# Optimization experiments

Measured on AMD Instinct MI355X. Metric: run time of the kernel, lower is better.

Reference implementation:

```python
import jax, jax.numpy as jnp
from jax import lax
import numpy as np

N, K, QK, W = 10, 10, 150, 128
D = 256
HID = 100
CHANS = [1, 16, 32, 64, 128, 256]
STRIDES = [2, 2, 1, 1, 1]
ITERS = 3
BN_EPS = 1e-5


def setup_inputs() -> dict:
    key = jax.random.key(0)
    ks = jax.random.split(key, 12)
    inp = {
        "support": jax.random.normal(ks[0], (N, K, 1, W, W), jnp.float32),
        "query": jax.random.normal(ks[1], (QK, 1, W, W), jnp.float32),
    }
    for i in range(5):
        inp[f"conv_w{i}"] = jax.random.normal(ks[2 + i], (CHANS[i + 1], CHANS[i], 3, 3), jnp.float32) * 0.05
        inp[f"bn_g{i}"] = jnp.ones((CHANS[i + 1],), jnp.float32)
        inp[f"bn_b{i}"] = jnp.zeros((CHANS[i + 1],), jnp.float32)
    inp["trans_w"] = jax.random.normal(ks[8], (D, D), jnp.float32) * 0.05
    inp["trans_b"] = jnp.zeros((D,), jnp.float32)
    inp["bil_w"] = jax.random.normal(ks[9], (HID, D, D), jnp.float32) * 0.02
    inp["score_w"] = jax.random.normal(ks[10], (1, HID), jnp.float32) * 0.1
    inp["score_b"] = jnp.zeros((1,), jnp.float32)
    return inp


def _block(x, w, g, b, s):
    # Conv2d(k=3, pad=1, stride=s, no bias) -> BatchNorm(eval: mean=0, var=1) -> ReLU -> MaxPool2d(2)
    x = lax.conv_general_dilated(x, w, (s, s), ((1, 1), (1, 1)),
                                 dimension_numbers=('NCHW', 'OIHW', 'NCHW'))
    scale = (g / jnp.sqrt(1.0 + BN_EPS))[None, :, None, None]
    x = jax.nn.relu(x * scale + b[None, :, None, None])
    return lax.reduce_window(x, -jnp.inf, lax.max, (1, 1, 2, 2), (1, 1, 2, 2), 'VALID')


def reference(support, query,
              conv_w0, conv_w1, conv_w2, conv_w3, conv_w4,
              bn_g0, bn_g1, bn_g2, bn_g3, bn_g4,
              bn_b0, bn_b1, bn_b2, bn_b3, bn_b4,
              trans_w, trans_b, bil_w, score_w, score_b):
    n, k = support.shape[0], support.shape[1]
    qk = query.shape[0]
    w = support.shape[3]

    ws = [conv_w0, conv_w1, conv_w2, conv_w3, conv_w4]
    gs = [bn_g0, bn_g1, bn_g2, bn_g3, bn_g4]
    bs = [bn_b0, bn_b1, bn_b2, bn_b3, bn_b4]

    # run the conv backbone on support+query jointly (BN is per-sample in eval mode)
    x = jnp.concatenate([support.reshape(n * k, 1, w, w), query], axis=0)
    for cw, g, b, s in zip(ws, gs, bs, STRIDES):
        x = _block(x, cw, g, b, s)
    feats = x.reshape(x.shape[0], -1)              # (n*k + qk, 256); spatial is 1x1
    sup = feats[:n * k].reshape(n, k, -1)          # (n, k, d)
    q = feats[n * k:]                              # (qk, d)

    # dynamic routing: Transformer(e) is recomputed each iter on the same input -> hoist
    e = sup @ trans_w.T + trans_b                  # (n, k, d)
    b0 = jnp.zeros((n, k), sup.dtype)

    def step(bb, _):
        dcoef = jax.nn.softmax(bb, axis=1)[:, :, None]   # (n, k, 1)
        c = (dcoef * e).sum(axis=1)                      # (n, d)
        cn = jnp.sqrt((c * c).sum(axis=1, keepdims=True))
        c = c * (cn / (cn * cn + 1.0))                   # squash: ||c||^2/(||c||^2+1)/||c||
        db = (c[:, None, :] * e).sum(axis=2)             # (n, k)
        return bb + db, c

    _, cs = lax.scan(step, b0, None, length=ITERS)
    proto = cs[-1]                                  # (n, d)

    # NTN: bilinear score for every (query, proto) pair, exploiting the pair structure
    t1 = jnp.einsum('nc,hce->nhe', proto, bil_w)    # (n, HID, d)
    v = jnp.einsum('nhe,qe->qnh', t1, q)            # (qk, n, HID)
    s = jax.nn.relu(v) @ score_w[0] + score_b[0]    # (qk, n)
    return jax.nn.log_softmax(s, axis=1)
```

## Files before the change

### kernel.cpp

```cpp
#include <hip/hip_runtime.h>
#include <math.h>


#define BN_SCALE rsqrtf(1.0f + 1e-5f)

#define OFF_FEATS 0
#define OFF_E     64000
#define OFF_S     89600
#define OFF_T1    91136
#define OFF_PROTO 347136
#define OFF_W1T   349696
#define OFF_W2T   354304
#define OFF_W3T   372736
#define OFF_W4T   446464
#define OFF_TWT   741376

__global__ void k_prep(const float* __restrict__ w1, const float* __restrict__ w2,
                       const float* __restrict__ w3, const float* __restrict__ w4,
                       const float* __restrict__ tw, float* __restrict__ ws) {
  float* w1t = ws + OFF_W1T;
  float* w2t = ws + OFF_W2T;
  float* w3t = ws + OFF_W3T;
  float* w4t = ws + OFF_W4T;
  float* twt = ws + OFF_TWT;
  int i = blockIdx.x * 256 + threadIdx.x;
  if (i < 4608) {
    int oc = i & 31; int r = i >> 5; int tap = r % 9; int ic = r / 9;
    w1t[i] = w1[(oc * 16 + ic) * 9 + tap];
  } else if (i < 23040) {
    int j = i - 4608;
    int oc = j & 63; int r = j >> 6; int tap = r % 9; int ic = r / 9;
    w2t[j] = w2[(oc * 32 + ic) * 9 + tap];
  } else if (i < 96768) {
    int j = i - 23040;
    int oc = j & 127; int r = j >> 7; int tap = r % 9; int ic = r / 9;
    w3t[j] = w3[(oc * 64 + ic) * 9 + tap];
  } else if (i < 391680) {
    int j = i - 96768;
    int oc = j & 255; int r = j >> 8; int tap = r % 9; int ic = r / 9;
    w4t[j] = w4[(oc * 128 + ic) * 9 + tap];
  } else if (i < 457216) {
    int j = i - 391680;
    int d = j >> 8, c = j & 255;
    twt[j] = tw[c * 256 + d];
  } else if (i < 713216) {
    ws[OFF_T1 + (i - 457216)] = 0.f;
  } else if (i < 714716) {
    ws[OFF_S + (i - 713216)] = 0.f;
  }
}

__global__ void __launch_bounds__(1024, 4)
k_main(const float* __restrict__ sup, const float* __restrict__ qry,
       const float* __restrict__ w0, const float* __restrict__ g0, const float* __restrict__ b0,
       const float* __restrict__ g1, const float* __restrict__ b1,
       const float* __restrict__ g2, const float* __restrict__ b2,
       const float* __restrict__ g3, const float* __restrict__ b3,
       const float* __restrict__ g4, const float* __restrict__ b4,
       const float* __restrict__ tb, float* __restrict__ ws,
       float* __restrict__ feats_g, float* __restrict__ e_buf) {
  __shared__ __align__(16) float S[38404];
  const float* w1t = ws + OFF_W1T;
  const float* w2t = ws + OFF_W2T;
  const float* w3t = ws + OFF_W3T;
  const float* w4t = ws + OFF_W4T;
  const float* twt = ws + OFF_TWT;
  const int img = blockIdx.x;
  const int t = threadIdx.x;
  const int lane = t & 63, wid = t >> 6;
  float* sa1 = S;
  float* sa2 = S + 4096;
  float* sa3 = S + 7424;
  float* sft = S + 7936;
  float* a0p = S + 8580;
  float* RED = S + 8580;
  float* L1R = S + 28164;

  const float* in = (img < 100) ? (sup + (size_t)img * 16384)
                                : (qry + (size_t)(img - 100) * 16384);

  {
    float4* S4 = (float4*)S;
    const float4 z4 = make_float4(0.f, 0.f, 0.f, 0.f);
    for (int i = t; i < 7041; i += 1024) S4[i] = z4;
  }
  __syncthreads();

  {
    const int ocp = wid & 7;
    const int rhalf = wid >> 3;
    const int oc0 = 2 * ocp, oc1 = oc0 + 1;
    float wv0[9], wv1[9];
#pragma unroll
    for (int k = 0; k < 9; k++) { wv0[k] = w0[oc0 * 9 + k]; wv1[k] = w0[oc1 * 9 + k]; }
    const float sc0 = g0[oc0] * BN_SCALE, bs0 = b0[oc0];
    const float sc1 = g0[oc1] * BN_SCALE, bs1 = b0[oc1];
#pragma unroll
    for (int it2 = 0; it2 < 2; it2++) {
      const int s2 = rhalf * 128 + it2 * 64 + lane;
      const int pr = s2 >> 3, pcq = s2 & 7;
      float ac0[2][8], ac1[2][8];
#pragma unroll
      for (int j = 0; j < 8; j++) {
        ac0[0][j] = 0.f; ac0[1][j] = 0.f; ac1[0][j] = 0.f; ac1[1][j] = 0.f;
      }
#pragma unroll
      for (int d = 0; d < 5; d++) {
        const int ir = 4 * pr - 1 + d;
        float x[17];
        if (ir >= 0) {
          const float* rp = in + ir * 128 + 16 * pcq;
          float4 q0 = ((const float4*)rp)[0];
          float4 q1 = ((const float4*)rp)[1];
          float4 q2 = ((const float4*)rp)[2];
          float4 q3 = ((const float4*)rp)[3];
          x[0] = (pcq > 0) ? rp[-1] : 0.f;
          x[1] = q0.x;  x[2] = q0.y;  x[3] = q0.z;  x[4] = q0.w;
          x[5] = q1.x;  x[6] = q1.y;  x[7] = q1.z;  x[8] = q1.w;
          x[9] = q2.x;  x[10] = q2.y; x[11] = q2.z; x[12] = q2.w;
          x[13] = q3.x; x[14] = q3.y; x[15] = q3.z; x[16] = q3.w;
        } else {
#pragma unroll
          for (int k = 0; k < 17; k++) x[k] = 0.f;
        }
        if (d <= 2) {
          const int b9 = d * 3;
#pragma unroll
          for (int j = 0; j < 8; j++) {
            ac0[0][j] = fmaf(x[2 * j + 2], wv0[b9 + 2],
                        fmaf(x[2 * j + 1], wv0[b9 + 1],
                        fmaf(x[2 * j],     wv0[b9],     ac0[0][j])));
            ac1[0][j] = fmaf(x[2 * j + 2], wv1[b9 + 2],
                        fmaf(x[2 * j + 1], wv1[b9 + 1],
                        fmaf(x[2 * j],     wv1[b9],     ac1[0][j])));
          }
        }
        if (d >= 2) {
          const int b9 = (d - 2) * 3;
#pragma unroll
          for (int j = 0; j < 8; j++) {
            ac0[1][j] = fmaf(x[2 * j + 2], wv0[b9 + 2],
                        fmaf(x[2 * j + 1], wv0[b9 + 1],
                        fmaf(x[2 * j],     wv0[b9],     ac0[1][j])));
            ac1[1][j] = fmaf(x[2 * j + 2], wv1[b9 + 2],
                        fmaf(x[2 * j + 1], wv1[b9 + 1],
                        fmaf(x[2 * j],     wv1[b9],     ac1[1][j])));
          }
        }
      }
      {
        float v[4];
#pragma unroll
        for (int p = 0; p < 4; p++) {
          float m = fmaf(ac0[0][2 * p], sc0, bs0);
          m = fmaxf(m, fmaf(ac0[0][2 * p + 1], sc0, bs0));
          m = fmaxf(m, fmaf(ac0[1][2 * p], sc0, bs0));
          m = fmaxf(m, fmaf(ac0[1][2 * p + 1], sc0, bs0));
          v[p] = fmaxf(m, 0.f);
        }
        *(float4*)(a0p + oc0 * 1224 + (pr + 1) * 36 + 4 * pcq) =
            make_float4(v[0], v[1], v[2], v[3]);
#pragma unroll
        for (int p = 0; p < 4; p++) {
          float m = fmaf(ac1[0][2 * p], sc1, bs1);
          m = fmaxf(m, fmaf(ac1[0][2 * p + 1], sc1, bs1));
          m = fmaxf(m, fmaf(ac1[1][2 * p], sc1, bs1));
          m = fmaxf(m, fmaf(ac1[1][2 * p + 1], sc1, bs1));
          v[p] = fmaxf(m, 0.f);
        }
        *(float4*)(a0p + oc1 * 1224 + (pr + 1) * 36 + 4 * pcq) =
            make_float4(v[0], v[1], v[2], v[3]);
      }
    }
  }
  __syncthreads();

  {
    const int pos = t & 63, py = pos >> 3, px = pos & 7;
    const int ocg = (t >> 6) & 7, icg = t >> 9;
    float acc[4][4];
#pragma unroll
    for (int j = 0; j < 4; j++)
#pragma unroll
      for (int p = 0; p < 4; p++) acc[j][p] = 0.f;
    const int ic0 = icg * 8;
    for (int ii = 0; ii < 8; ii++) {
      const int ic = ic0 + ii;
      float4 wq[9];
#pragma unroll
      for (int k = 0; k < 9; k++)
        wq[k] = *(const float4*)(w1t + (ic * 9 + k) * 32 + 4 * ocg);
      float win[25];
      const float* rb = a0p + ic * 1224 + 4 * py * 36 + 4 * px;
#pragma unroll
      for (int d = 0; d < 5; d++) {
        const float* rp = rb + d * 36;
        win[d * 5 + 0] = rp[-1];
        float4 r4 = *(const float4*)rp;
        win[d * 5 + 1] = r4.x; win[d * 5 + 2] = r4.y;
        win[d * 5 + 3] = r4.z; win[d * 5 + 4] = r4.w;
      }
#pragma unroll
      for (int cy = 0; cy < 2; cy++)
#pragma unroll
        for (int cx = 0; cx < 2; cx++) {
          const int p = cy * 2 + cx;
#pragma unroll
          for (int ky = 0; ky < 3; ky++)
#pragma unroll
            for (int kx = 0; kx < 3; kx++) {
              const float iv = win[(2 * cy + ky) * 5 + (2 * cx + kx)];
              const float4 wk = wq[ky * 3 + kx];
              acc[0][p] = fmaf(iv, wk.x, acc[0][p]);
              acc[1][p] = fmaf(iv, wk.y, acc[1][p]);
              acc[2][p] = fmaf(iv, wk.z, acc[2][p]);
              acc[3][p] = fmaf(iv, wk.w, acc[3][p]);
            }
        }
    }
    const int slot = ocg * 64 + pos;
    if (icg == 1) {
      float* wp2 = L1R + slot * 20;
#pragma unroll
      for (int j = 0; j < 4; j++)
        *(float4*)(wp2 + j * 4) = make_float4(acc[j][0], acc[j][1], acc[j][2], acc[j][3]);
    }
    __syncthreads();
    if (icg == 0) {
      const float* rp2 = L1R + slot * 20;
#pragma unroll
      for (int j = 0; j < 4; j++) {
        float4 o = *(const float4*)(rp2 + j * 4);
        const int oc = ocg * 4 + j;
        const float sc = g1[oc] * BN_SCALE, bsj = b1[oc];
        float m = fmaf(acc[j][0] + o.x, sc, bsj);
        m = fmaxf(m, fmaf(acc[j][1] + o.y, sc, bsj));
        m = fmaxf(m, fmaf(acc[j][2] + o.z, sc, bsj));
        m = fmaxf(m, fmaf(acc[j][3] + o.w, sc, bsj));
        sa1[oc * 124 + (py + 1) * 12 + (px + 1)] = fmaxf(m, 0.f);
      }
    }
  }
  __syncthreads();

  {
    int oc = t & 63, icg = (t >> 6) & 3, pg = t >> 8;
    int pgy = pg >> 1, pgx = pg & 1;
    float acc[16];
#pragma unroll
    for (int p = 0; p < 16; p++) acc[p] = 0.f;
    float wc[9];
    {
      const float* wp = w2t + (icg * 8) * 576 + oc;
#pragma unroll
      for (int k = 0; k < 9; k++) wc[k] = wp[k * 64];
    }
    for (int ii = 0; ii < 8; ii++) {
      int ic = icg * 8 + ii;
      float wn[9];
      if (ii < 7) {
        const float* wp = w2t + (ic + 1) * 576 + oc;
#pragma unroll
        for (int k = 0; k < 9; k++) wn[k] = wp[k * 64];
      }
      float win[6][6];
      const float* bp = sa1 + ic * 124 + 4 * pgy * 12 + 4 * pgx;
#pragma unroll
      for (int d = 0; d < 6; d++) {
        float4 u = *(const float4*)(bp + d * 12);
        float2 v = *(const float2*)(bp + d * 12 + 4);
        win[d][0] = u.x; win[d][1] = u.y; win[d][2] = u.z; win[d][3] = u.w;
        win[d][4] = v.x; win[d][5] = v.y;
      }
#pragma unroll
      for (int u = 0; u < 4; u++)
#pragma unroll
        for (int v = 0; v < 4; v++) {
          float c = acc[u * 4 + v];
#pragma unroll
          for (int ky = 0; ky < 3; ky++)
#pragma unroll
            for (int kx = 0; kx < 3; kx++)
              c = fmaf(win[u + ky][v + kx], wc[ky * 3 + kx], c);
          acc[u * 4 + v] = c;
        }
      if (ii < 7) {
#pragma unroll
        for (int k = 0; k < 9; k++) wc[k] = wn[k];
      }
    }
#pragma unroll
    for (int j = 0; j < 16; j++) RED[j * 1024 + icg * 256 + pg * 64 + oc] = acc[j];
  }
  __syncthreads();
  if (t < 256) {
    int oc = t & 63, pg = t >> 6;
    int pgy = pg >> 1, pgx = pg & 1;
    float sc = g2[oc] * BN_SCALE, bsj = b2[oc];
#pragma unroll
    for (int cy = 0; cy < 2; cy++)
#pragma unroll
      for (int cx = 0; cx < 2; cx++) {
        float m = -1e30f;
#pragma unroll
        for (int a = 0; a < 2; a++)
#pragma unroll
          for (int b = 0; b < 2; b++) {
            int j = (2 * cy + a) * 4 + (2 * cx + b);
            float v = RED[j * 1024 + pg * 64 + oc] + RED[j * 1024 + 256 + pg * 64 + oc]
                    + RED[j * 1024 + 512 + pg * 64 + oc] + RED[j * 1024 + 768 + pg * 64 + oc];
            m = fmaxf(m, fmaf(v, sc, bsj));
          }
        sa2[oc * 52 + (1 + 2 * pgy + cy) * 8 + (1 + 2 * pgx + cx)] = fmaxf(m, 0.f);
      }
  }
  __syncthreads();

  {
    int oc = t & 127, icg = t >> 7;
    float acc[16];
#pragma unroll
    for (int p = 0; p < 16; p++) acc[p] = 0.f;
    float wc[9];
    {
      const float* wp = w3t + (icg * 8) * 1152 + oc;
#pragma unroll
      for (int k = 0; k < 9; k++) wc[k] = wp[k * 128];
    }
    for (int ii = 0; ii < 8; ii++) {
      int ic = icg * 8 + ii;
      float wn[9];
      if (ii < 7) {
        const float* wp = w3t + (ic + 1) * 1152 + oc;
#pragma unroll
        for (int k = 0; k < 9; k++) wn[k] = wp[k * 128];
      }
      float win[6][6];
      const float* bp = sa2 + ic * 52;
#pragma unroll
      for (int d = 0; d < 6; d++) {
        float4 u = *(const float4*)(bp + d * 8);
        float2 v = *(const float2*)(bp + d * 8 + 4);
        win[d][0] = u.x; win[d][1] = u.y; win[d][2] = u.z; win[d][3] = u.w;
        win[d][4] = v.x; win[d][5] = v.y;
      }
#pragma unroll
      for (int u = 0; u < 4; u++)
#pragma unroll
        for (int v = 0; v < 4; v++) {
          float c = acc[u * 4 + v];
#pragma unroll
          for (int ky = 0; ky < 3; ky++)
#pragma unroll
            for (int kx = 0; kx < 3; kx++)
              c = fmaf(win[u + ky][v + kx], wc[ky * 3 + kx], c);
          acc[u * 4 + v] = c;
        }
      if (ii < 7) {
#pragma unroll
        for (int k = 0; k < 9; k++) wc[k] = wn[k];
      }
    }
#pragma unroll
    for (int j = 0; j < 16; j++) RED[j * 1024 + icg * 128 + oc] = acc[j];
  }
  __syncthreads();
  if (t < 512) {
    int oc = t & 127, pp = t >> 7;
    int py = pp >> 1, px = pp & 1;
    float sc = g3[oc] * BN_SCALE, bsj = b3[oc];
    float m = -1e30f;
#pragma unroll
    for (int a = 0; a < 2; a++)
#pragma unroll
      for (int b = 0; b < 2; b++) {
        int j = (2 * py + a) * 4 + (2 * px + b);
        float v = 0.f;
#pragma unroll
        for (int g = 0; g < 8; g++) v += RED[j * 1024 + g * 128 + oc];
        m = fmaxf(m, fmaf(v, sc, bsj));
      }
    sa3[oc * 4 + pp] = fmaxf(m, 0.f);
  }
  __syncthreads();

  {
    int oc = t & 255, icq = t >> 8;
    float acc[4] = {0.f, 0.f, 0.f, 0.f};
    float wc[9];
    {
      const float* wp = w4t + (icq * 32) * 2304 + oc;
#pragma unroll
      for (int k = 0; k < 9; k++) wc[k] = wp[k * 256];
    }
    for (int ii = 0; ii < 32; ii++) {
      int ic = icq * 32 + ii;
      float wn[9];
      if (ii < 31) {
        const float* wp = w4t + (ic + 1) * 2304 + oc;
#pragma unroll
        for (int k = 0; k < 9; k++) wn[k] = wp[k * 256];
      }
      float4 iv = *(const float4*)(sa3 + ic * 4);
#pragma unroll
      for (int py = 0; py < 2; py++)
#pragma unroll
        for (int px = 0; px < 2; px++) {
          float c = acc[py * 2 + px];
          c = fmaf(iv.x, wc[(1 - py) * 3 + (1 - px)], c);
          c = fmaf(iv.y, wc[(1 - py) * 3 + (2 - px)], c);
          c = fmaf(iv.z, wc[(2 - py) * 3 + (1 - px)], c);
          c = fmaf(iv.w, wc[(2 - py) * 3 + (2 - px)], c);
          acc[py * 2 + px] = c;
        }
      if (ii < 31) {
#pragma unroll
        for (int k = 0; k < 9; k++) wc[k] = wn[k];
      }
    }
    if (icq) {
#pragma unroll
      for (int p = 0; p < 4; p++) RED[((icq - 1) * 256 + oc) * 4 + p] = acc[p];
    }
    __syncthreads();
    if (icq == 0) {
      float sc = g4[oc] * BN_SCALE, bsj = b4[oc];
      float m = -1e30f;
#pragma unroll
      for (int p = 0; p < 4; p++) {
        float v = acc[p] + RED[oc * 4 + p] + RED[(256 + oc) * 4 + p] + RED[(512 + oc) * 4 + p];
        m = fmaxf(m, fmaf(v, sc, bsj));
      }
      float r = fmaxf(m, 0.f);
      sft[oc] = r;
      feats_g[(size_t)img * 256 + oc] = r;
    }
  }
  __syncthreads();

  if (img < 100) {
    int c = t & 255, dq = t >> 8;
    float acc = 0.f;
    float wv = twt[(dq * 64) * 256 + c];
#pragma unroll 4
    for (int ii = 0; ii < 64; ii++) {
      int d = dq * 64 + ii;
      float wnext = (ii < 63) ? twt[(d + 1) * 256 + c] : 0.f;
      acc = fmaf(sft[d], wv, acc);
      wv = wnext;
    }
    if (dq) RED[(dq - 1) * 256 + c] = acc;
    __syncthreads();
    if (dq == 0)
      e_buf[img * 256 + c] = acc + RED[c] + RED[256 + c] + RED[512 + c] + tb[c];
  }
}

__global__ void k_routing(const float* __restrict__ e, float* __restrict__ proto) {
  int n = blockIdx.x;
  __shared__ float sb[10], sdc[10], red[4], red2[40], sfc[1];
  int t = threadIdx.x;
  int lane = t & 63, wid = t >> 6;
  float ek[10];
#pragma unroll
  for (int k = 0; k < 10; k++) ek[k] = e[n * 2560 + k * 256 + t];
  if (t < 10) sb[t] = 0.f;
  __syncthreads();
  float cd = 0.f;
  for (int iter = 0; iter < 3; iter++) {
    if (t == 0) {
      float mx = sb[0];
      for (int k = 1; k < 10; k++) mx = fmaxf(mx, sb[k]);
      float sum = 0.f;
      for (int k = 0; k < 10; k++) { float ex = expf(sb[k] - mx); sdc[k] = ex; sum += ex; }
      float inv = 1.f / sum;
      for (int k = 0; k < 10; k++) sdc[k] *= inv;
    }
    __syncthreads();
    cd = 0.f;
#pragma unroll
    for (int k = 0; k < 10; k++) cd = fmaf(sdc[k], ek[k], cd);
    float ss = cd * cd;
#pragma unroll
    for (int off = 32; off > 0; off >>= 1) ss += __shfl_down(ss, off, 64);
    if (lane == 0) red[wid] = ss;
    __syncthreads();
    if (t == 0) {
      float tot = red[0] + red[1] + red[2] + red[3];
      sfc[0] = sqrtf(tot) / (tot + 1.f);
    }
    __syncthreads();
    cd *= sfc[0];
    float pr[10];
#pragma unroll
    for (int k = 0; k < 10; k++) pr[k] = cd * ek[k];
#pragma unroll
    for (int off = 32; off > 0; off >>= 1)
#pragma unroll
      for (int k = 0; k < 10; k++) pr[k] += __shfl_down(pr[k], off, 64);
    if (lane == 0)
#pragma unroll
      for (int k = 0; k < 10; k++) red2[k * 4 + wid] = pr[k];
    __syncthreads();
    if (t < 10) sb[t] += red2[t * 4] + red2[t * 4 + 1] + red2[t * 4 + 2] + red2[t * 4 + 3];
    __syncthreads();
  }
  proto[n * 256 + t] = cd;
}

__global__ void k_t1(const float* __restrict__ proto, const float* __restrict__ bw,
                     float* __restrict__ t1) {
  __shared__ float pt[384];
  const int b = blockIdx.x;
  const int h = b >> 3, c0 = (b & 7) * 32;
  const int t = threadIdx.x;
  for (int i = t; i < 320; i += 256) {
    int n = i >> 5, cl = i & 31;
    pt[cl * 12 + n] = proto[n * 256 + c0 + cl];
  }
  __syncthreads();
  float acc[10];
#pragma unroll
  for (int n = 0; n < 10; n++) acc[n] = 0.f;
  const float* wp = bw + (size_t)h * 65536 + (size_t)c0 * 256 + t;
#pragma unroll 4
  for (int cl = 0; cl < 32; cl++) {
    float wv = wp[(size_t)cl * 256];
    float4 p0 = *(const float4*)(pt + cl * 12);
    float4 p1 = *(const float4*)(pt + cl * 12 + 4);
    float2 p2 = *(const float2*)(pt + cl * 12 + 8);
    acc[0] = fmaf(p0.x, wv, acc[0]); acc[1] = fmaf(p0.y, wv, acc[1]);
    acc[2] = fmaf(p0.z, wv, acc[2]); acc[3] = fmaf(p0.w, wv, acc[3]);
    acc[4] = fmaf(p1.x, wv, acc[4]); acc[5] = fmaf(p1.y, wv, acc[5]);
    acc[6] = fmaf(p1.z, wv, acc[6]); acc[7] = fmaf(p1.w, wv, acc[7]);
    acc[8] = fmaf(p2.x, wv, acc[8]); acc[9] = fmaf(p2.y, wv, acc[9]);
  }
#pragma unroll
  for (int n = 0; n < 10; n++)
    atomicAdd(&t1[((size_t)n * 100 + h) * 256 + t], acc[n]);
}

__global__ void k_score(const float* __restrict__ t1, const float* __restrict__ qf,
                        const float* __restrict__ sw, float* __restrict__ s) {
  __shared__ float sq[256];
  __shared__ float vb[2000];
  const int q = blockIdx.x >> 1, hh = blockIdx.x & 1;
  const int t = threadIdx.x;
  const int sl = t & 3, quad = t >> 2;
  sq[t] = qf[q * 256 + t];
  __syncthreads();
  const float4* qr = (const float4*)sq;
#pragma unroll
  for (int j = 0; j < 8; j++) {
    int lr = quad + 64 * j;
    if (lr < 500) {
      int n = lr / 50, hl = lr % 50;
      const float4* row = (const float4*)(t1 + ((size_t)(n * 100 + hh * 50 + hl)) * 256);
      float acc = 0.f;
#pragma unroll
      for (int d = 0; d < 16; d++) {
        float4 a = row[d * 4 + sl];
        float4 b = qr[d * 4 + sl];
        acc += a.x * b.x + a.y * b.y + a.z * b.z + a.w * b.w;
      }
      vb[lr * 4 + sl] = acc;
    }
  }
  __syncthreads();
  if (t < 10) {
    float sum = 0.f;
    for (int hl = 0; hl < 50; hl++) {
      int lr = t * 50 + hl;
      float d = vb[lr * 4] + vb[lr * 4 + 1] + vb[lr * 4 + 2] + vb[lr * 4 + 3];
      sum = fmaf(fmaxf(d, 0.f), sw[hh * 50 + hl], sum);
    }
    atomicAdd(&s[q * 10 + t], sum);
  }
}

__global__ void k_lsm(const float* __restrict__ s, const float* __restrict__ sbp,
                      float* __restrict__ out) {
  int q = threadIdx.x;
  if (q >= 150) return;
  float sb0 = sbp[0];
  float v[10];
  float mx = -1e30f;
#pragma unroll
  for (int n = 0; n < 10; n++) {
    v[n] = s[q * 10 + n] + sb0;
    mx = fmaxf(mx, v[n]);
  }
  float sum = 0.f;
#pragma unroll
  for (int n = 0; n < 10; n++) sum += expf(v[n] - mx);
  float lse = mx + logf(sum);
#pragma unroll
  for (int n = 0; n < 10; n++) out[q * 10 + n] = v[n] - lse;
}

extern "C" void kernel_launch(void* const* d_in, const int* in_sizes, int n_in,
                              void* d_out, int out_size, void* d_ws, size_t ws_size,
                              hipStream_t stream) {
  const float* support = (const float*)d_in[0];
  const float* query   = (const float*)d_in[1];
  const float* conv_w[5]; const float* bn_g[5]; const float* bn_b[5];
  for (int i = 0; i < 5; i++) {
    conv_w[i] = (const float*)d_in[2 + 3 * i];
    bn_g[i]   = (const float*)d_in[3 + 3 * i];
    bn_b[i]   = (const float*)d_in[4 + 3 * i];
  }
  const float* trans_w = (const float*)d_in[17];
  const float* trans_b = (const float*)d_in[18];
  const float* bil_w   = (const float*)d_in[19];
  const float* score_w = (const float*)d_in[20];
  const float* score_b = (const float*)d_in[21];
  float* out = (float*)d_out;
  float* ws = (float*)d_ws;

  float* feats = ws + OFF_FEATS;
  float* e_buf = ws + OFF_E;
  float* s_buf = ws + OFF_S;
  float* t1    = ws + OFF_T1;
  float* proto = ws + OFF_PROTO;

  k_prep<<<2793, 256, 0, stream>>>(conv_w[1], conv_w[2], conv_w[3], conv_w[4],
                                   trans_w, ws);
  k_main<<<250, 1024, 0, stream>>>(support, query,
                                   conv_w[0], bn_g[0], bn_b[0],
                                   bn_g[1], bn_b[1], bn_g[2], bn_b[2],
                                   bn_g[3], bn_b[3], bn_g[4], bn_b[4],
                                   trans_b, ws, feats, e_buf);
  k_routing<<<10, 256, 0, stream>>>(e_buf, proto);
  k_t1<<<800, 256, 0, stream>>>(proto, bil_w, t1);
  k_score<<<300, 256, 0, stream>>>(t1, feats + 100 * 256, score_w, s_buf);
  k_lsm<<<1, 256, 0, stream>>>(s_buf, score_b, out);
}
```

Baseline: 210.4 us.

## Replace LDS cross-thread reductions with wavefront shuffle reductions in conv stages

Each conv stage and the transformer projection now remap threads so that the input-channel split lives within one wavefront, and partial sums are combined with __shfl_xor instead of being written to a shared-memory reduction buffer and re-read after a barrier. This removes the RED/L1R scratch, shrinking LDS from about 150KB to about 110KB, and drops several __syncthreads. The prep kernel now reads weights coalesced and scatters the transposed writes. Register-level weight prefetching in layers 2 and 3 is removed. The interleaved channel split changes the memory access pattern and the summation order.

```diff
diff --git a/kernel.cpp b/kernel.cpp
--- a/kernel.cpp
+++ b/kernel.cpp
@@ -25,24 +25,28 @@
   float* twt = ws + OFF_TWT;
   int i = blockIdx.x * 256 + threadIdx.x;
   if (i < 4608) {
-    int oc = i & 31; int r = i >> 5; int tap = r % 9; int ic = r / 9;
-    w1t[i] = w1[(oc * 16 + ic) * 9 + tap];
+    int oc = i / 144, r = i % 144;
+    int ic = r / 9, tap = r % 9;
+    w1t[(ic * 9 + tap) * 32 + oc] = w1[i];
   } else if (i < 23040) {
-    int j = i - 4608;
-    int oc = j & 63; int r = j >> 6; int tap = r % 9; int ic = r / 9;
-    w2t[j] = w2[(oc * 32 + ic) * 9 + tap];
+    int m = i - 4608;
+    int oc = m / 288, r = m % 288;
+    int ic = r / 9, tap = r % 9;
+    w2t[(ic * 9 + tap) * 64 + oc] = w2[m];
   } else if (i < 96768) {
-    int j = i - 23040;
-    int oc = j & 127; int r = j >> 7; int tap = r % 9; int ic = r / 9;
-    w3t[j] = w3[(oc * 64 + ic) * 9 + tap];
+    int m = i - 23040;
+    int oc = m / 576, r = m % 576;
+    int ic = r / 9, tap = r % 9;
+    w3t[(ic * 9 + tap) * 128 + oc] = w3[m];
   } else if (i < 391680) {
-    int j = i - 96768;
-    int oc = j & 255; int r = j >> 8; int tap = r % 9; int ic = r / 9;
-    w4t[j] = w4[(oc * 128 + ic) * 9 + tap];
+    int m = i - 96768;
+    int oc = m / 1152, r = m % 1152;
+    int ic = r / 9, tap = r % 9;
+    w4t[(ic * 9 + tap) * 256 + oc] = w4[m];
   } else if (i < 457216) {
-    int j = i - 391680;
-    int d = j >> 8, c = j & 255;
-    twt[j] = tw[c * 256 + d];
+    int m = i - 391680;
+    int r = m >> 8, s = m & 255;
+    twt[s * 256 + r] = tw[m];
   } else if (i < 713216) {
     ws[OFF_T1 + (i - 457216)] = 0.f;
   } else if (i < 714716) {
@@ -59,7 +63,7 @@
        const float* __restrict__ g4, const float* __restrict__ b4,
        const float* __restrict__ tb, float* __restrict__ ws,
        float* __restrict__ feats_g, float* __restrict__ e_buf) {
-  __shared__ __align__(16) float S[38404];
+  __shared__ __align__(16) float S[28164];
   const float* w1t = ws + OFF_W1T;
   const float* w2t = ws + OFF_W2T;
   const float* w3t = ws + OFF_W3T;
@@ -73,8 +77,6 @@
   float* sa3 = S + 7424;
   float* sft = S + 7936;
   float* a0p = S + 8580;
-  float* RED = S + 8580;
-  float* L1R = S + 28164;
 
   const float* in = (img < 100) ? (sup + (size_t)img * 16384)
                                 : (qry + (size_t)(img - 100) * 16384);
@@ -176,41 +178,41 @@
   __syncthreads();
 
   {
-    const int pos = t & 63, py = pos >> 3, px = pos & 7;
-    const int ocg = (t >> 6) & 7, icg = t >> 9;
+    const int w = t >> 6;
+    const int ocg = w >> 1, posh = w & 1;
+    const int posl = lane & 31, icg = lane >> 5;
+    const int pos = posh * 32 + posl;
+    const int py = pos >> 3, px = pos & 7;
     float acc[4][4];
 #pragma unroll
     for (int j = 0; j < 4; j++)
 #pragma unroll
       for (int p = 0; p < 4; p++) acc[j][p] = 0.f;
-    const int ic0 = icg * 8;
+#pragma unroll 2
     for (int ii = 0; ii < 8; ii++) {
-      const int ic = ic0 + ii;
-      float4 wq[9];
-#pragma unroll
-      for (int k = 0; k < 9; k++)
-        wq[k] = *(const float4*)(w1t + (ic * 9 + k) * 32 + 4 * ocg);
+      const int ic = icg + 2 * ii;
       float win[25];
       const float* rb = a0p + ic * 1224 + 4 * py * 36 + 4 * px;
 #pragma unroll
       for (int d = 0; d < 5; d++) {
-        const float* rp = rb + d * 36;
-        win[d * 5 + 0] = rp[-1];
-        float4 r4 = *(const float4*)rp;
-        win[d * 5 + 1] = r4.x; win[d * 5 + 2] = r4.y;
-        win[d * 5 + 3] = r4.z; win[d * 5 + 4] = r4.w;
-      }
-#pragma unroll
-      for (int cy = 0; cy < 2; cy++)
-#pragma unroll
-        for (int cx = 0; cx < 2; cx++) {
-          const int p = cy * 2 + cx;
-#pragma unroll
-          for (int ky = 0; ky < 3; ky++)
-#pragma unroll
-            for (int kx = 0; kx < 3; kx++) {
+        float4 a = *(const float4*)(rb + d * 36 - 4);
+        float4 b = *(const float4*)(rb + d * 36);
+        win[d * 5 + 0] = a.w;
+        win[d * 5 + 1] = b.x; win[d * 5 + 2] = b.y;
+        win[d * 5 + 3] = b.z; win[d * 5 + 4] = b.w;
+      }
+      const float* wb = w1t + ic * 288 + 4 * ocg;
+#pragma unroll
+      for (int ky = 0; ky < 3; ky++)
+#pragma unroll
+        for (int kx = 0; kx < 3; kx++) {
+          const float4 wk = *(const float4*)(wb + (ky * 3 + kx) * 32);
+#pragma unroll
+          for (int cy = 0; cy < 2; cy++)
+#pragma unroll
+            for (int cx = 0; cx < 2; cx++) {
+              const int p = cy * 2 + cx;
               const float iv = win[(2 * cy + ky) * 5 + (2 * cx + kx)];
-              const float4 wk = wq[ky * 3 + kx];
               acc[0][p] = fmaf(iv, wk.x, acc[0][p]);
               acc[1][p] = fmaf(iv, wk.y, acc[1][p]);
               acc[2][p] = fmaf(iv, wk.z, acc[2][p]);
@@ -218,25 +220,20 @@
             }
         }
     }
-    const int slot = ocg * 64 + pos;
-    if (icg == 1) {
-      float* wp2 = L1R + slot * 20;
-#pragma unroll
-      for (int j = 0; j < 4; j++)
-        *(float4*)(wp2 + j * 4) = make_float4(acc[j][0], acc[j][1], acc[j][2], acc[j][3]);
-    }
-    __syncthreads();
+#pragma unroll
+    for (int j = 0; j < 4; j++)
+#pragma unroll
+      for (int p = 0; p < 4; p++)
+        acc[j][p] += __shfl_xor(acc[j][p], 32);
     if (icg == 0) {
-      const float* rp2 = L1R + slot * 20;
 #pragma unroll
       for (int j = 0; j < 4; j++) {
-        float4 o = *(const float4*)(rp2 + j * 4);
         const int oc = ocg * 4 + j;
         const float sc = g1[oc] * BN_SCALE, bsj = b1[oc];
-        float m = fmaf(acc[j][0] + o.x, sc, bsj);
-        m = fmaxf(m, fmaf(acc[j][1] + o.y, sc, bsj));
-        m = fmaxf(m, fmaf(acc[j][2] + o.z, sc, bsj));
-        m = fmaxf(m, fmaf(acc[j][3] + o.w, sc, bsj));
+        float m = fmaf(acc[j][0], sc, bsj);
+        m = fmaxf(m, fmaf(acc[j][1], sc, bsj));
+        m = fmaxf(m, fmaf(acc[j][2], sc, bsj));
+        m = fmaxf(m, fmaf(acc[j][3], sc, bsj));
         sa1[oc * 124 + (py + 1) * 12 + (px + 1)] = fmaxf(m, 0.f);
       }
     }
@@ -244,25 +241,20 @@
   __syncthreads();
 
   {
-    int oc = t & 63, icg = (t >> 6) & 3, pg = t >> 8;
-    int pgy = pg >> 1, pgx = pg & 1;
+    const int w = t >> 6;
+    const int pg = w >> 2, ocb = w & 3;
+    const int ocl = lane & 15, icg = lane >> 4;
+    const int oc = ocb * 16 + ocl;
+    const int pgy = pg >> 1, pgx = pg & 1;
     float acc[16];
 #pragma unroll
     for (int p = 0; p < 16; p++) acc[p] = 0.f;
-    float wc[9];
-    {
-      const float* wp = w2t + (icg * 8) * 576 + oc;
+    for (int ii = 0; ii < 8; ii++) {
+      const int ic = icg + 4 * ii;
+      float wc[9];
+      const float* wp = w2t + ic * 576 + oc;
 #pragma unroll
       for (int k = 0; k < 9; k++) wc[k] = wp[k * 64];
-    }
-    for (int ii = 0; ii < 8; ii++) {
-      int ic = icg * 8 + ii;
-      float wn[9];
-      if (ii < 7) {
-        const float* wp = w2t + (ic + 1) * 576 + oc;
-#pragma unroll
-        for (int k = 0; k < 9; k++) wn[k] = wp[k * 64];
-      }
       float win[6][6];
       const float* bp = sa1 + ic * 124 + 4 * pgy * 12 + 4 * pgx;
 #pragma unroll
@@ -284,57 +276,43 @@
               c = fmaf(win[u + ky][v + kx], wc[ky * 3 + kx], c);
           acc[u * 4 + v] = c;
         }
-      if (ii < 7) {
-#pragma unroll
-        for (int k = 0; k < 9; k++) wc[k] = wn[k];
-      }
-    }
-#pragma unroll
-    for (int j = 0; j < 16; j++) RED[j * 1024 + icg * 256 + pg * 64 + oc] = acc[j];
-  }
-  __syncthreads();
-  if (t < 256) {
-    int oc = t & 63, pg = t >> 6;
-    int pgy = pg >> 1, pgx = pg & 1;
-    float sc = g2[oc] * BN_SCALE, bsj = b2[oc];
-#pragma unroll
-    for (int cy = 0; cy < 2; cy++)
-#pragma unroll
-      for (int cx = 0; cx < 2; cx++) {
-        float m = -1e30f;
-#pragma unroll
-        for (int a = 0; a < 2; a++)
-#pragma unroll
-          for (int b = 0; b < 2; b++) {
-            int j = (2 * cy + a) * 4 + (2 * cx + b);
-            float v = RED[j * 1024 + pg * 64 + oc] + RED[j * 1024 + 256 + pg * 64 + oc]
-                    + RED[j * 1024 + 512 + pg * 64 + oc] + RED[j * 1024 + 768 + pg * 64 + oc];
-            m = fmaxf(m, fmaf(v, sc, bsj));
-          }
-        sa2[oc * 52 + (1 + 2 * pgy + cy) * 8 + (1 + 2 * pgx + cx)] = fmaxf(m, 0.f);
-      }
+    }
+#pragma unroll
+    for (int p = 0; p < 16; p++) {
+      acc[p] += __shfl_xor(acc[p], 16);
+      acc[p] += __shfl_xor(acc[p], 32);
+    }
+    if (icg == 0) {
+      const float sc = g2[oc] * BN_SCALE, bsj = b2[oc];
+#pragma unroll
+      for (int cy = 0; cy < 2; cy++)
+#pragma unroll
+        for (int cx = 0; cx < 2; cx++) {
+          float m = -1e30f;
+#pragma unroll
+          for (int a = 0; a < 2; a++)
+#pragma unroll
+            for (int b = 0; b < 2; b++)
+              m = fmaxf(m, fmaf(acc[(2 * cy + a) * 4 + (2 * cx + b)], sc, bsj));
+          sa2[oc * 52 + (1 + 2 * pgy + cy) * 8 + (1 + 2 * pgx + cx)] = fmaxf(m, 0.f);
+        }
+    }
   }
   __syncthreads();
 
   {
-    int oc = t & 127, icg = t >> 7;
+    const int w = t >> 6;
+    const int ocl = lane & 7, icg = lane >> 3;
+    const int oc = w * 8 + ocl;
     float acc[16];
 #pragma unroll
     for (int p = 0; p < 16; p++) acc[p] = 0.f;
-    float wc[9];
-    {
-      const float* wp = w3t + (icg * 8) * 1152 + oc;
+    for (int ii = 0; ii < 8; ii++) {
+      const int ic = icg + 8 * ii;
+      float wc[9];
+      const float* wp = w3t + ic * 1152 + oc;
 #pragma unroll
       for (int k = 0; k < 9; k++) wc[k] = wp[k * 128];
-    }
-    for (int ii = 0; ii < 8; ii++) {
-      int ic = icg * 8 + ii;
-      float wn[9];
-      if (ii < 7) {
-        const float* wp = w3t + (ic + 1) * 1152 + oc;
-#pragma unroll
-        for (int k = 0; k < 9; k++) wn[k] = wp[k * 128];
-      }
       float win[6][6];
       const float* bp = sa2 + ic * 52;
 #pragma unroll
@@ -356,48 +334,48 @@
               c = fmaf(win[u + ky][v + kx], wc[ky * 3 + kx], c);
           acc[u * 4 + v] = c;
         }
-      if (ii < 7) {
-#pragma unroll
-        for (int k = 0; k < 9; k++) wc[k] = wn[k];
-      }
-    }
-#pragma unroll
-    for (int j = 0; j < 16; j++) RED[j * 1024 + icg * 128 + oc] = acc[j];
-  }
-  __syncthreads();
-  if (t < 512) {
-    int oc = t & 127, pp = t >> 7;
-    int py = pp >> 1, px = pp & 1;
-    float sc = g3[oc] * BN_SCALE, bsj = b3[oc];
-    float m = -1e30f;
-#pragma unroll
-    for (int a = 0; a < 2; a++)
-#pragma unroll
-      for (int b = 0; b < 2; b++) {
-        int j = (2 * py + a) * 4 + (2 * px + b);
-        float v = 0.f;
-#pragma unroll
-        for (int g = 0; g < 8; g++) v += RED[j * 1024 + g * 128 + oc];
-        m = fmaxf(m, fmaf(v, sc, bsj));
-      }
-    sa3[oc * 4 + pp] = fmaxf(m, 0.f);
+    }
+#pragma unroll
+    for (int p = 0; p < 16; p++) {
+      acc[p] += __shfl_xor(acc[p], 8);
+      acc[p] += __shfl_xor(acc[p], 16);
+      acc[p] += __shfl_xor(acc[p], 32);
+    }
+    if (icg == 0) {
+      const float sc = g3[oc] * BN_SCALE, bsj = b3[oc];
+      float v[4];
+#pragma unroll
+      for (int pp = 0; pp < 4; pp++) {
+        const int py = pp >> 1, px = pp & 1;
+        float m = -1e30f;
+#pragma unroll
+        for (int a = 0; a < 2; a++)
+#pragma unroll
+          for (int b = 0; b < 2; b++)
+            m = fmaxf(m, fmaf(acc[(2 * py + a) * 4 + (2 * px + b)], sc, bsj));
+        v[pp] = fmaxf(m, 0.f);
+      }
+      *(float4*)(sa3 + oc * 4) = make_float4(v[0], v[1], v[2], v[3]);
+    }
   }
   __syncthreads();
 
   {
-    int oc = t & 255, icq = t >> 8;
+    const int w = t >> 6;
+    const int ocl = lane & 15, icq = lane >> 4;
+    const int oc = w * 16 + ocl;
     float acc[4] = {0.f, 0.f, 0.f, 0.f};
     float wc[9];
     {
-      const float* wp = w4t + (icq * 32) * 2304 + oc;
+      const float* wp = w4t + icq * 2304 + oc;
 #pragma unroll
       for (int k = 0; k < 9; k++) wc[k] = wp[k * 256];
     }
     for (int ii = 0; ii < 32; ii++) {
-      int ic = icq * 32 + ii;
+      const int ic = icq + 4 * ii;
       float wn[9];
       if (ii < 31) {
-        const float* wp = w4t + (ic + 1) * 2304 + oc;
+        const float* wp = w4t + (ic + 4) * 2304 + oc;
 #pragma unroll
         for (int k = 0; k < 9; k++) wn[k] = wp[k * 256];
       }
@@ -418,19 +396,16 @@
         for (int k = 0; k < 9; k++) wc[k] = wn[k];
       }
     }
-    if (icq) {
-#pragma unroll
-      for (int p = 0; p < 4; p++) RED[((icq - 1) * 256 + oc) * 4 + p] = acc[p];
-    }
-    __syncthreads();
+#pragma unroll
+    for (int p = 0; p < 4; p++) {
+      acc[p] += __shfl_xor(acc[p], 16);
+      acc[p] += __shfl_xor(acc[p], 32);
+    }
     if (icq == 0) {
-      float sc = g4[oc] * BN_SCALE, bsj = b4[oc];
+      const float sc = g4[oc] * BN_SCALE, bsj = b4[oc];
       float m = -1e30f;
 #pragma unroll
-      for (int p = 0; p < 4; p++) {
-        float v = acc[p] + RED[oc * 4 + p] + RED[(256 + oc) * 4 + p] + RED[(512 + oc) * 4 + p];
-        m = fmaxf(m, fmaf(v, sc, bsj));
-      }
+      for (int p = 0; p < 4; p++) m = fmaxf(m, fmaf(acc[p], sc, bsj));
       float r = fmaxf(m, 0.f);
       sft[oc] = r;
       feats_g[(size_t)img * 256 + oc] = r;
@@ -439,20 +414,18 @@
   __syncthreads();
 
   if (img < 100) {
-    int c = t & 255, dq = t >> 8;
+    const int w = t >> 6;
+    const int c = w * 16 + (lane & 15);
+    const int dq = lane >> 4;
     float acc = 0.f;
-    float wv = twt[(dq * 64) * 256 + c];
 #pragma unroll 4
     for (int ii = 0; ii < 64; ii++) {
-      int d = dq * 64 + ii;
-      float wnext = (ii < 63) ? twt[(d + 1) * 256 + c] : 0.f;
-      acc = fmaf(sft[d], wv, acc);
-      wv = wnext;
-    }
-    if (dq) RED[(dq - 1) * 256 + c] = acc;
-    __syncthreads();
-    if (dq == 0)
-      e_buf[img * 256 + c] = acc + RED[c] + RED[256 + c] + RED[512 + c] + tb[c];
+      const int d = dq + 4 * ii;
+      acc = fmaf(sft[d], twt[d * 256 + c], acc);
+    }
+    acc += __shfl_xor(acc, 16);
+    acc += __shfl_xor(acc, 32);
+    if (dq == 0) e_buf[img * 256 + c] = acc + tb[c];
   }
 }
 
```

Result: no change. 214.2 us (+1.8%).
